# Kernel optimization log

Measured on AMD Instinct MI355X. Metric: run time of the kernel, lower is better.

## Reference

```python
import jax, jax.numpy as jnp
import numpy as np

N = 10000      # nodes
E = 320000     # edges (before self-loops)
IN = 256       # in_channels
HID = 128      # hidden_channels
HEADS = 4
OUT = 64       # out_channels
G = 64         # graphs in batch
NEG_SLOPE = 0.2


def setup_inputs() -> dict:
    key = jax.random.key(0)
    ks = jax.random.split(key, 12)
    s = lambda fan: 1.0 / np.sqrt(fan)
    x = jax.random.normal(ks[0], (N, IN), jnp.float32)
    edge_index = jax.random.randint(ks[1], (2, E), 0, N, dtype=jnp.int32)
    batch = jnp.sort(jax.random.randint(ks[2], (N,), 0, G, dtype=jnp.int32))
    # layer 0: GATConv(IN -> HID, heads=HEADS, concat)
    W1 = jax.random.normal(ks[3], (IN, HEADS * HID), jnp.float32) * s(IN)
    a1s = jax.random.normal(ks[4], (HEADS, HID), jnp.float32) * s(HID)
    a1d = jax.random.normal(ks[5], (HEADS, HID), jnp.float32) * s(HID)
    b1 = jnp.zeros((HEADS * HID,), jnp.float32)
    # layer 1: GATConv(HEADS*HID -> HID, heads=1)
    W2 = jax.random.normal(ks[6], (HEADS * HID, HID), jnp.float32) * s(HEADS * HID)
    a2s = jax.random.normal(ks[7], (1, HID), jnp.float32) * s(HID)
    a2d = jax.random.normal(ks[8], (1, HID), jnp.float32) * s(HID)
    b2 = jnp.zeros((HID,), jnp.float32)
    fc_w = jax.random.normal(ks[9], (HID, OUT), jnp.float32) * s(HID)
    fc_b = jnp.zeros((OUT,), jnp.float32)
    return dict(x=x, edge_index=edge_index, batch=batch, W1=W1, a1s=a1s,
                a1d=a1d, b1=b1, W2=W2, a2s=a2s, a2d=a2d, b2=b2,
                fc_w=fc_w, fc_b=fc_b)


def _gat_conv(x, src, dst, W, a_src, a_dst, b, heads):
    """PyG GATConv (concat=True, self-loops already in src/dst)."""
    n = x.shape[0]
    h = (x @ W).reshape(n, heads, -1)                     # [N,H,C]
    alpha_s = jnp.einsum('nhc,hc->nh', h, a_src)          # [N,H]
    alpha_d = jnp.einsum('nhc,hc->nh', h, a_dst)
    e = jax.nn.leaky_relu(alpha_s[src] + alpha_d[dst], NEG_SLOPE)  # [Etot,H]
    # per-destination-node segment softmax
    e = e - jax.ops.segment_max(e, dst, num_segments=n)[dst]
    e = jnp.exp(e)
    denom = jax.ops.segment_sum(e, dst, num_segments=n)[dst] + 1e-16
    alpha = e / denom
    out = jax.ops.segment_sum(h[src] * alpha[:, :, None], dst, num_segments=n)
    return out.reshape(n, -1) + b


def reference(x, edge_index, batch, W1, a1s, a1d, b1, W2, a2s, a2d, b2, fc_w, fc_b):
    loops = jnp.arange(N, dtype=edge_index.dtype)
    ei = jnp.concatenate([edge_index, jnp.stack([loops, loops])], axis=1)
    src, dst = ei[0], ei[1]
    h = jax.nn.relu(_gat_conv(x, src, dst, W1, a1s, a1d, b1, HEADS))
    h = jax.nn.relu(_gat_conv(h, src, dst, W2, a2s, a2d, b2, 1))
    # global_mean_pool over graph ids
    counts = jax.ops.segment_sum(jnp.ones((N, 1), h.dtype), batch, num_segments=G)
    pooled = jax.ops.segment_sum(h, batch, num_segments=G) / jnp.maximum(counts, 1.0)
    return pooled @ fc_w + fc_b
```

## Files before the change

### kernel.cpp

```cpp
#include <hip/hip_runtime.h>
#include <math.h>

#define NN 10000
#define EE 320000
#define GG 64
#define NT 157
#define NPAD (NT * 64)

#define NB 64
#define CH (EE / NB)
#define HSTR 10240

typedef __attribute__((ext_vector_type(8))) short short8;
typedef __attribute__((ext_vector_type(4))) float f32x4;

__device__ __forceinline__ float leaky(float x) { return x >= 0.f ? x : 0.2f * x; }

__device__ __forceinline__ unsigned f2bf(float f) {
  unsigned u = __float_as_uint(f);
  return (u + 0x7fffu + ((u >> 16) & 1u)) >> 16;
}
__device__ __forceinline__ float bflo(unsigned v) { return __uint_as_float(v << 16); }
__device__ __forceinline__ float bfhi(unsigned v) { return __uint_as_float(v & 0xffff0000u); }

__device__ void histA_body(int blk, const int* __restrict__ ei,
                           int* __restrict__ hist2d,
                           ushort* __restrict__ lrank) {
  __shared__ int lh[NN];
  for (int i = threadIdx.x; i < NN; i += 256) lh[i] = 0;
  __syncthreads();
  const int base = blk * CH;
  for (int i = threadIdx.x; i < CH; i += 256) {
    int d = ei[EE + base + i];
    int r = atomicAdd(&lh[d], 1);
    lrank[base + i] = (ushort)r;
  }
  __syncthreads();
  int* hrow = hist2d + (size_t)blk * HSTR;
  for (int i = threadIdx.x; i < NN; i += 256) hrow[i] = lh[i];
}

__device__ __forceinline__ void s1_body(int sb, const int* __restrict__ hist2d,
                                        int* __restrict__ off2d,
                                        int* __restrict__ total) {
  int t = sb * 256 + threadIdx.x;
  if (t >= NN) return;
  int run = 0;
#pragma unroll 8
  for (int b = 0; b < NB; b++) {
    int v = hist2d[(size_t)b * HSTR + t];
    off2d[(size_t)b * HSTR + t] = run;
    run += v;
  }
  total[t] = run;
}

__device__ void scan_body(const int* __restrict__ total,
                          int* __restrict__ rowstart) {
  __shared__ int part[256];
  const int tid = threadIdx.x;
  const int PER = 40;
  int base = tid * PER;
  int local[PER];
  int s = 0;
#pragma unroll
  for (int i = 0; i < PER; i++) {
    int idx = base + i;
    int v = (idx < NN) ? total[idx] : 0;
    local[i] = s;
    s += v;
  }
  part[tid] = s;
  __syncthreads();
  for (int off = 1; off < 256; off <<= 1) {
    int v = (tid >= off) ? part[tid - off] : 0;
    __syncthreads();
    part[tid] += v;
    __syncthreads();
  }
  int pre = (tid == 0) ? 0 : part[tid - 1];
#pragma unroll
  for (int i = 0; i < PER; i++) {
    int idx = base + i;
    if (idx < NN) rowstart[idx] = pre + local[i];
  }
  if (tid == 255) rowstart[NN] = part[255];
}

__device__ __forceinline__ void fillB_body(int bx, const int* __restrict__ ei,
                                           const int* __restrict__ rowstart,
                                           const int* __restrict__ off2d,
                                           const ushort* __restrict__ lrank,
                                           int* __restrict__ esrc) {
  int e = bx * 256 + threadIdx.x;
  if (e >= EE) return;
  int d = ei[EE + e];
  int s = ei[e];
  int blk = e / CH;
  int pos = rowstart[d] + off2d[(size_t)blk * HSTR + d] + (int)lrank[e];
  esrc[pos] = s;
}

#define PX_ITEMS (NN * 256 / 8)
#define PW1 (512 * 256)
#define PW2 (128 * 512)
#define PACK_BLKS ((PX_ITEMS + PW1 + PW2) / 256)

__device__ __forceinline__ void pack_body(int pb, const float* __restrict__ x,
                                          const float* __restrict__ W1,
                                          const float* __restrict__ W2,
                                          uint4* __restrict__ xb,
                                          ushort* __restrict__ w1hi,
                                          ushort* __restrict__ w2hi) {
  int idx = pb * 256 + threadIdx.x;
  if (idx < PX_ITEMS) {
    const float4* xf = (const float4*)x;
    float4 a = xf[idx * 2], b = xf[idx * 2 + 1];
    uint4 o;
    o.x = f2bf(a.x) | (f2bf(a.y) << 16);
    o.y = f2bf(a.z) | (f2bf(a.w) << 16);
    o.z = f2bf(b.x) | (f2bf(b.y) << 16);
    o.w = f2bf(b.z) | (f2bf(b.w) << 16);
    xb[idx] = o;
  } else if (idx < PX_ITEMS + PW1) {
    int i = idx - PX_ITEMS;
    int c = i >> 8, k = i & 255;
    w1hi[i] = (ushort)f2bf(W1[(size_t)k * 512 + c]);
  } else if (idx < PX_ITEMS + PW1 + PW2) {
    int i = idx - PX_ITEMS - PW1;
    int c = i >> 9, k = i & 511;
    w2hi[i] = (ushort)f2bf(W2[(size_t)k * 128 + c]);
  }
}

__device__ __forceinline__ void gstart_body(int gb, const int* __restrict__ batch,
                                            int* __restrict__ gstart) {
  int i = gb * 256 + threadIdx.x;
  if (i >= NN) return;
  int b = batch[i];
  int prev = (i == 0) ? -1 : batch[i - 1];
  for (int g = prev + 1; g <= b; g++) gstart[g] = i;
  if (i == NN - 1)
    for (int g = b + 1; g <= GG; g++) gstart[g] = NN;
}

#define ZERO_BLKS ((NN * 4 + 255) / 256)
__device__ __forceinline__ void zero_body(int zb, float* __restrict__ as1,
                                          float* __restrict__ ad1,
                                          float* __restrict__ as2,
                                          float* __restrict__ ad2) {
  int i = zb * 256 + threadIdx.x;
  if (i < NN) { as2[i] = 0.f; ad2[i] = 0.f; }
  if (i < NN * 4) { as1[i] = 0.f; ad1[i] = 0.f; }
}

__device__ void gemmt_body(int chblk, int nodeblk,
                           const ushort* __restrict__ ab,
                           const ushort* __restrict__ whi,
                           unsigned* __restrict__ op,
                           const float* __restrict__ avs,
                           const float* __restrict__ avd,
                           float* __restrict__ as_out,
                           float* __restrict__ ad_out,
                           int K, int C) {
  const int lane = threadIdx.x & 63;
  const int wave = threadIdx.x >> 6;
  const int l15 = lane & 15;
  const int kg = lane >> 4;
  const int ch0 = chblk * 64 + wave * 16;
  const int node0 = nodeblk * 64;
  const ushort* arow_hi = whi + (size_t)(ch0 + l15) * K + kg * 8;
  const ushort* brow = ab + (size_t)(node0 + l15) * K + kg * 8;
  f32x4 acc[4];
#pragma unroll
  for (int f = 0; f < 4; f++) acc[f] = (f32x4){0.f, 0.f, 0.f, 0.f};
  for (int k0 = 0; k0 < K; k0 += 32) {
    short8 ah = *(const short8*)(arow_hi + k0);
#pragma unroll
    for (int f = 0; f < 4; f++) {
      short8 bv = *(const short8*)(brow + (size_t)f * 16 * K + k0);
      acc[f] = __builtin_amdgcn_mfma_f32_16x16x32_bf16(ah, bv, acc[f], 0, 0, 0);
    }
  }
  const int chw = ch0 + kg * 4;
  const int head = ch0 >> 7;
  const int H = C >> 7;
  const float4 s4 = *(const float4*)(avs + chw);
  const float4 d4 = *(const float4*)(avd + chw);
#pragma unroll
  for (int f = 0; f < 4; f++) {
    int node = node0 + f * 16 + l15;
    unsigned u0 = f2bf(acc[f][0]) | (f2bf(acc[f][1]) << 16);
    unsigned u1 = f2bf(acc[f][2]) | (f2bf(acc[f][3]) << 16);
    *(uint2*)(op + (size_t)node * (C >> 1) + (chw >> 1)) = make_uint2(u0, u1);
    float ss = acc[f][0] * s4.x + acc[f][1] * s4.y + acc[f][2] * s4.z + acc[f][3] * s4.w;
    float sd = acc[f][0] * d4.x + acc[f][1] * d4.y + acc[f][2] * d4.z + acc[f][3] * d4.w;
    ss += __shfl_xor(ss, 16, 64); ss += __shfl_xor(ss, 32, 64);
    sd += __shfl_xor(sd, 16, 64); sd += __shfl_xor(sd, 32, 64);
    if (kg == 0 && node < NN) {
      atomicAdd(&as_out[node * H + head], ss);
      atomicAdd(&ad_out[node * H + head], sd);
    }
  }
}

#define FILL_BLKS 1250
#define GST_BLKS 40
__global__ __launch_bounds__(256) void fusedA_k(const int* __restrict__ ei,
                                                int* __restrict__ hist2d,
                                                ushort* __restrict__ lrank,
                                                const float* __restrict__ x,
                                                const float* __restrict__ W1,
                                                const float* __restrict__ W2,
                                                uint4* __restrict__ xb,
                                                ushort* __restrict__ w1hi,
                                                ushort* __restrict__ w2hi,
                                                const int* __restrict__ batch,
                                                int* __restrict__ gstart,
                                                float* __restrict__ as1,
                                                float* __restrict__ ad1,
                                                float* __restrict__ as2,
                                                float* __restrict__ ad2) {
  int bx = blockIdx.x;
  if (bx < NB) histA_body(bx, ei, hist2d, lrank);
  else if (bx < NB + PACK_BLKS)
    pack_body(bx - NB, x, W1, W2, xb, w1hi, w2hi);
  else if (bx < NB + PACK_BLKS + GST_BLKS)
    gstart_body(bx - NB - PACK_BLKS, batch, gstart);
  else
    zero_body(bx - NB - PACK_BLKS - GST_BLKS, as1, ad1, as2, ad2);
}

__global__ __launch_bounds__(256) void fusedB_k(const int* __restrict__ hist2d,
                                                int* __restrict__ off2d,
                                                int* __restrict__ total,
                                                const ushort* __restrict__ xb,
                                                const ushort* __restrict__ w1hi,
                                                unsigned* __restrict__ h1p,
                                                const float* __restrict__ a1s,
                                                const float* __restrict__ a1d,
                                                float* __restrict__ as1,
                                                float* __restrict__ ad1) {
  int bx = blockIdx.x;
  if (bx < GST_BLKS) { s1_body(bx, hist2d, off2d, total); return; }
  int lb = bx - GST_BLKS;
  int ch = lb % 3, nb = lb / 3;
  gemmt_body(ch, nb, xb, w1hi, h1p, a1s, a1d, as1, ad1, 256, 512);
}

__global__ __launch_bounds__(256) void fusedC_k(const int* __restrict__ total,
                                                int* __restrict__ rowstart,
                                                const ushort* __restrict__ xb,
                                                const ushort* __restrict__ w1hi,
                                                unsigned* __restrict__ h1p,
                                                const float* __restrict__ a1s,
                                                const float* __restrict__ a1d,
                                                float* __restrict__ as1,
                                                float* __restrict__ ad1) {
  int bx = blockIdx.x;
  if (bx == 0) { scan_body(total, rowstart); return; }
  int lb = bx - 1;
  int ch = 3 + lb % 3, nb = lb / 3;
  gemmt_body(ch, nb, xb, w1hi, h1p, a1s, a1d, as1, ad1, 256, 512);
}

__global__ __launch_bounds__(256) void fusedD_k(const int* __restrict__ ei,
                                                const int* __restrict__ rowstart,
                                                const int* __restrict__ off2d,
                                                const ushort* __restrict__ lrank,
                                                int* __restrict__ esrc,
                                                const ushort* __restrict__ xb,
                                                const ushort* __restrict__ w1hi,
                                                unsigned* __restrict__ h1p,
                                                const float* __restrict__ a1s,
                                                const float* __restrict__ a1d,
                                                float* __restrict__ as1,
                                                float* __restrict__ ad1) {
  int bx = blockIdx.x;
  if (bx < FILL_BLKS) { fillB_body(bx, ei, rowstart, off2d, lrank, esrc); return; }
  int lb = bx - FILL_BLKS;
  int ch = 6 + (lb & 1), nb = lb >> 1;
  gemmt_body(ch, nb, xb, w1hi, h1p, a1s, a1d, as1, ad1, 256, 512);
}

__global__ __launch_bounds__(256) void gemmt_k(const ushort* __restrict__ ab,
                                               const ushort* __restrict__ whi,
                                               unsigned* __restrict__ op,
                                               const float* __restrict__ avs,
                                               const float* __restrict__ avd,
                                               float* __restrict__ as_out,
                                               float* __restrict__ ad_out,
                                               int K, int C) {
  gemmt_body(blockIdx.x, blockIdx.y, ab, whi, op, avs, avd, as_out, ad_out, K, C);
}

#define AGG1_FMA8(W_, HV_)                          \
  acc0.x = fmaf(W_, bflo(HV_.x), acc0.x);           \
  acc0.y = fmaf(W_, bfhi(HV_.x), acc0.y);           \
  acc0.z = fmaf(W_, bflo(HV_.y), acc0.z);           \
  acc0.w = fmaf(W_, bfhi(HV_.y), acc0.w);           \
  acc1.x = fmaf(W_, bflo(HV_.z), acc1.x);           \
  acc1.y = fmaf(W_, bfhi(HV_.z), acc1.y);           \
  acc1.z = fmaf(W_, bflo(HV_.w), acc1.z);           \
  acc1.w = fmaf(W_, bfhi(HV_.w), acc1.w);

__global__ __launch_bounds__(256) void agg1_k(const int* __restrict__ rowstart,
                                              const int* __restrict__ esrc,
                                              const float* __restrict__ as,
                                              const float* __restrict__ ad,
                                              const ushort* __restrict__ h1p,
                                              const float* __restrict__ b1,
                                              uint4* __restrict__ o1b) {
  const int lane = threadIdx.x & 63;
  const int wid = threadIdx.x >> 6;
  const int n = blockIdx.x * 4 + wid;
  const int beg = rowstart[n];
  const int deg = rowstart[n + 1] - beg;
  const int tot = deg + 1;
  const float4* as4 = (const float4*)as;
  const float4 adv = ((const float4*)ad)[n];
  const int head = lane >> 4;

  __shared__ float wlds_all[4][256];
  float* wlds = wlds_all[wid];

  int s0 = n;
  float4 e0 = make_float4(-1e30f, -1e30f, -1e30f, -1e30f);
  if (lane < tot) {
    if (lane < deg) s0 = esrc[beg + lane];
    float4 av = as4[s0];
    e0.x = leaky(av.x + adv.x); e0.y = leaky(av.y + adv.y);
    e0.z = leaky(av.z + adv.z); e0.w = leaky(av.w + adv.w);
  }
  float4 mx = e0;
  for (int i = lane + 64; i < tot; i += 64) {
    int s = (i < deg) ? esrc[beg + i] : n;
    float4 av = as4[s];
    mx.x = fmaxf(mx.x, leaky(av.x + adv.x));
    mx.y = fmaxf(mx.y, leaky(av.y + adv.y));
    mx.z = fmaxf(mx.z, leaky(av.z + adv.z));
    mx.w = fmaxf(mx.w, leaky(av.w + adv.w));
  }
#pragma unroll
  for (int off = 32; off >= 1; off >>= 1) {
    mx.x = fmaxf(mx.x, __shfl_xor(mx.x, off, 64));
    mx.y = fmaxf(mx.y, __shfl_xor(mx.y, off, 64));
    mx.z = fmaxf(mx.z, __shfl_xor(mx.z, off, 64));
    mx.w = fmaxf(mx.w, __shfl_xor(mx.w, off, 64));
  }
  float4 sm;
  sm.x = __expf(e0.x - mx.x); sm.y = __expf(e0.y - mx.y);
  sm.z = __expf(e0.z - mx.z); sm.w = __expf(e0.w - mx.w);
  for (int i = lane + 64; i < tot; i += 64) {
    int s = (i < deg) ? esrc[beg + i] : n;
    float4 av = as4[s];
    sm.x += __expf(leaky(av.x + adv.x) - mx.x);
    sm.y += __expf(leaky(av.y + adv.y) - mx.y);
    sm.z += __expf(leaky(av.z + adv.z) - mx.z);
    sm.w += __expf(leaky(av.w + adv.w) - mx.w);
  }
#pragma unroll
  for (int off = 32; off >= 1; off >>= 1) {
    sm.x += __shfl_xor(sm.x, off, 64);
    sm.y += __shfl_xor(sm.y, off, 64);
    sm.z += __shfl_xor(sm.z, off, 64);
    sm.w += __shfl_xor(sm.w, off, 64);
  }
  float4 inv;
  inv.x = 1.f / (sm.x + 1e-16f); inv.y = 1.f / (sm.y + 1e-16f);
  inv.z = 1.f / (sm.z + 1e-16f); inv.w = 1.f / (sm.w + 1e-16f);

  float4 acc0 = make_float4(0.f, 0.f, 0.f, 0.f);
  float4 acc1 = make_float4(0.f, 0.f, 0.f, 0.f);
  const char* hb = (const char*)h1p + (size_t)lane * 16;

  for (int base = 0; base < tot; base += 64) {
    int sl;
    float4 wl;
    if (base == 0) {
      sl = s0;
      wl.x = __expf(e0.x - mx.x) * inv.x;
      wl.y = __expf(e0.y - mx.y) * inv.y;
      wl.z = __expf(e0.z - mx.z) * inv.z;
      wl.w = __expf(e0.w - mx.w) * inv.w;
    } else {
      int i = base + lane;
      sl = n;
      wl = make_float4(0.f, 0.f, 0.f, 0.f);
      if (i < tot) {
        if (i < deg) sl = esrc[beg + i];
        float4 av = as4[sl];
        wl.x = __expf(leaky(av.x + adv.x) - mx.x) * inv.x;
        wl.y = __expf(leaky(av.y + adv.y) - mx.y) * inv.y;
        wl.z = __expf(leaky(av.z + adv.z) - mx.z) * inv.z;
        wl.w = __expf(leaky(av.w + adv.w) - mx.w) * inv.w;
      }
    }
    *(float4*)&wlds[lane * 4] = wl;
    int m = min(64, tot - base);
    int j = 0;
    for (; j + 4 <= m; j += 4) {
      int sA = __builtin_amdgcn_readlane(sl, j);
      int sB = __builtin_amdgcn_readlane(sl, j + 1);
      int sC = __builtin_amdgcn_readlane(sl, j + 2);
      int sD = __builtin_amdgcn_readlane(sl, j + 3);
      uint4 hA = *(const uint4*)(hb + (size_t)sA * 1024);
      uint4 hB = *(const uint4*)(hb + (size_t)sB * 1024);
      uint4 hC = *(const uint4*)(hb + (size_t)sC * 1024);
      uint4 hD = *(const uint4*)(hb + (size_t)sD * 1024);
      float wA = wlds[j * 4 + head];
      float wB = wlds[(j + 1) * 4 + head];
      float wC = wlds[(j + 2) * 4 + head];
      float wD = wlds[(j + 3) * 4 + head];
      AGG1_FMA8(wA, hA)
      AGG1_FMA8(wB, hB)
      AGG1_FMA8(wC, hC)
      AGG1_FMA8(wD, hD)
    }
    for (; j < m; j++) {
      int sA = __builtin_amdgcn_readlane(sl, j);
      float wA = wlds[j * 4 + head];
      uint4 hA = *(const uint4*)(hb + (size_t)sA * 1024);
      AGG1_FMA8(wA, hA)
    }
  }
  const float4* b4 = (const float4*)b1;
  float4 ba = b4[2 * lane], bb = b4[2 * lane + 1];
  float4 r0, r1;
  r0.x = fmaxf(acc0.x + ba.x, 0.f); r0.y = fmaxf(acc0.y + ba.y, 0.f);
  r0.z = fmaxf(acc0.z + ba.z, 0.f); r0.w = fmaxf(acc0.w + ba.w, 0.f);
  r1.x = fmaxf(acc1.x + bb.x, 0.f); r1.y = fmaxf(acc1.y + bb.y, 0.f);
  r1.z = fmaxf(acc1.z + bb.z, 0.f); r1.w = fmaxf(acc1.w + bb.w, 0.f);
  uint4 o;
  o.x = f2bf(r0.x) | (f2bf(r0.y) << 16);
  o.y = f2bf(r0.z) | (f2bf(r0.w) << 16);
  o.z = f2bf(r1.x) | (f2bf(r1.y) << 16);
  o.w = f2bf(r1.z) | (f2bf(r1.w) << 16);
  o1b[(size_t)n * 64 + lane] = o;
}

__global__ __launch_bounds__(256) void agg2_k(const int* __restrict__ rowstart,
                                              const int* __restrict__ esrc,
                                              const float* __restrict__ as,
                                              const float* __restrict__ ad,
                                              const ushort* __restrict__ h2p,
                                              const float* __restrict__ b2,
                                              float* __restrict__ out2) {
  const int lane = threadIdx.x & 63;
  const int wid = threadIdx.x >> 6;
  const int n = blockIdx.x * 4 + wid;
  const int beg = rowstart[n];
  const int deg = rowstart[n + 1] - beg;
  const int tot = deg + 1;
  const float adv = ad[n];

  __shared__ float wlds_all[4][64];
  float* wlds = wlds_all[wid];

  int s0 = n;
  float e0 = -1e30f;
  if (lane < tot) {
    if (lane < deg) s0 = esrc[beg + lane];
    e0 = leaky(as[s0] + adv);
  }
  float mx = e0;
  for (int i = lane + 64; i < tot; i += 64) {
    int s = (i < deg) ? esrc[beg + i] : n;
    mx = fmaxf(mx, leaky(as[s] + adv));
  }
#pragma unroll
  for (int off = 32; off >= 1; off >>= 1) mx = fmaxf(mx, __shfl_xor(mx, off, 64));
  float sm = __expf(e0 - mx);
  for (int i = lane + 64; i < tot; i += 64) {
    int s = (i < deg) ? esrc[beg + i] : n;
    sm += __expf(leaky(as[s] + adv) - mx);
  }
#pragma unroll
  for (int off = 32; off >= 1; off >>= 1) sm += __shfl_xor(sm, off, 64);
  float inv = 1.f / (sm + 1e-16f);

  float2 acc = make_float2(0.f, 0.f);
  const char* hb = (const char*)h2p + (size_t)lane * 4;
  for (int base = 0; base < tot; base += 64) {
    int sl;
    float wl;
    if (base == 0) {
      sl = s0;
      wl = __expf(e0 - mx) * inv;
    } else {
      int i = base + lane;
      sl = n; wl = 0.f;
      if (i < tot) {
        if (i < deg) sl = esrc[beg + i];
        wl = __expf(leaky(as[sl] + adv) - mx) * inv;
      }
    }
    wlds[lane] = wl;
    int m = min(64, tot - base);
    int j = 0;
    for (; j + 4 <= m; j += 4) {
      int sA = __builtin_amdgcn_readlane(sl, j);
      int sB = __builtin_amdgcn_readlane(sl, j + 1);
      int sC = __builtin_amdgcn_readlane(sl, j + 2);
      int sD = __builtin_amdgcn_readlane(sl, j + 3);
      unsigned hA = *(const unsigned*)(hb + (size_t)sA * 256);
      unsigned hB = *(const unsigned*)(hb + (size_t)sB * 256);
      unsigned hC = *(const unsigned*)(hb + (size_t)sC * 256);
      unsigned hD = *(const unsigned*)(hb + (size_t)sD * 256);
      float wA = wlds[j], wB = wlds[j + 1], wC = wlds[j + 2], wD = wlds[j + 3];
      acc.x = fmaf(wA, bflo(hA), acc.x);
      acc.y = fmaf(wA, bfhi(hA), acc.y);
      acc.x = fmaf(wB, bflo(hB), acc.x);
      acc.y = fmaf(wB, bfhi(hB), acc.y);
      acc.x = fmaf(wC, bflo(hC), acc.x);
      acc.y = fmaf(wC, bfhi(hC), acc.y);
      acc.x = fmaf(wD, bflo(hD), acc.x);
      acc.y = fmaf(wD, bfhi(hD), acc.y);
    }
    for (; j < m; j++) {
      int sA = __builtin_amdgcn_readlane(sl, j);
      float wA = wlds[j];
      unsigned hA = *(const unsigned*)(hb + (size_t)sA * 256);
      acc.x = fmaf(wA, bflo(hA), acc.x);
      acc.y = fmaf(wA, bfhi(hA), acc.y);
    }
  }
  float2 bb = ((const float2*)b2)[lane];
  float2 r;
  r.x = fmaxf(acc.x + bb.x, 0.f);
  r.y = fmaxf(acc.y + bb.y, 0.f);
  ((float2*)(out2 + (size_t)n * 128))[lane] = r;
}

__global__ __launch_bounds__(128) void poolfc_k(const int* __restrict__ gstart,
                                                const float* __restrict__ out2,
                                                const float* __restrict__ fcw,
                                                const float* __restrict__ fcb,
                                                float* __restrict__ out) {
  const int g = blockIdx.x;
  const int tid = threadIdx.x;
  const int beg = gstart[g], end = gstart[g + 1];
  const int cnt = end - beg;
  float acc = 0.f;
  int n = beg;
  for (; n + 4 <= end; n += 4) {
    float v0 = out2[(size_t)(n + 0) * 128 + tid];
    float v1 = out2[(size_t)(n + 1) * 128 + tid];
    float v2 = out2[(size_t)(n + 2) * 128 + tid];
    float v3 = out2[(size_t)(n + 3) * 128 + tid];
    acc += (v0 + v1) + (v2 + v3);
  }
  for (; n < end; n++) acc += out2[(size_t)n * 128 + tid];
  __shared__ float pg[128];
  pg[tid] = acc / (float)(cnt > 0 ? cnt : 1);
  __syncthreads();
  if (tid < 64) {
    float o = fcb[tid];
#pragma unroll 8
    for (int c = 0; c < 128; c++) o = fmaf(pg[c], fcw[c * 64 + tid], o);
    out[g * 64 + tid] = o;
  }
}

extern "C" void kernel_launch(void* const* d_in, const int* in_sizes, int n_in,
                              void* d_out, int out_size, void* d_ws, size_t ws_size,
                              hipStream_t stream) {
  const float* x   = (const float*)d_in[0];
  const int*   ei  = (const int*)d_in[1];
  const int*   bat = (const int*)d_in[2];
  const float* W1  = (const float*)d_in[3];
  const float* a1s = (const float*)d_in[4];
  const float* a1d = (const float*)d_in[5];
  const float* b1  = (const float*)d_in[6];
  const float* W2  = (const float*)d_in[7];
  const float* a2s = (const float*)d_in[8];
  const float* a2d = (const float*)d_in[9];
  const float* b2  = (const float*)d_in[10];
  const float* fcw = (const float*)d_in[11];
  const float* fcb = (const float*)d_in[12];
  float* out = (float*)d_out;

  char* ws = (char*)d_ws;
  size_t off = 0;
  auto alloc = [&](size_t bytes) -> void* {
    void* p = ws + off;
    off = (off + bytes + 255) & ~(size_t)255;
    return p;
  };

  int*   hist2d   = (int*)alloc((size_t)NB * HSTR * 4);
  int*   off2d    = (int*)alloc((size_t)NB * HSTR * 4);
  ushort* lrank   = (ushort*)alloc((size_t)EE * 2);
  int*   total    = (int*)alloc((size_t)NN * 4);
  int*   rowstart = (int*)alloc((size_t)(NN + 1) * 4);
  int*   esrc     = (int*)alloc((size_t)EE * 4);
  int*   gstart   = (int*)alloc((size_t)(GG + 1) * 4);
  ushort* xb      = (ushort*)alloc((size_t)NPAD * 256 * 2);
  ushort* w1hi    = (ushort*)alloc((size_t)512 * 256 * 2);
  ushort* w2hi    = (ushort*)alloc((size_t)128 * 512 * 2);
  ushort* h1p     = (ushort*)alloc((size_t)NPAD * 512 * 2);
  ushort* o1b     = (ushort*)alloc((size_t)NPAD * 512 * 2);
  ushort* h2p     = (ushort*)alloc((size_t)NPAD * 128 * 2);
  float* as1      = (float*)alloc((size_t)NN * 4 * 4);
  float* ad1      = (float*)alloc((size_t)NN * 4 * 4);
  float* as2      = (float*)alloc((size_t)NN * 4);
  float* ad2      = (float*)alloc((size_t)NN * 4);
  float* out2     = (float*)alloc((size_t)NN * 128 * 4);
  (void)ws_size; (void)in_sizes; (void)n_in; (void)out_size;

  fusedA_k<<<NB + PACK_BLKS + GST_BLKS + ZERO_BLKS, 256, 0, stream>>>(
      ei, hist2d, lrank, x, W1, W2, (uint4*)xb, w1hi, w2hi, bat, gstart,
      as1, ad1, as2, ad2);

  fusedB_k<<<GST_BLKS + 3 * NT, 256, 0, stream>>>(hist2d, off2d, total, xb, w1hi,
                                                  (unsigned*)h1p, a1s, a1d, as1, ad1);

  fusedC_k<<<1 + 3 * NT, 256, 0, stream>>>(total, rowstart, xb, w1hi,
                                           (unsigned*)h1p, a1s, a1d, as1, ad1);

  fusedD_k<<<FILL_BLKS + 2 * NT, 256, 0, stream>>>(ei, rowstart, off2d, lrank, esrc,
                                                   xb, w1hi, (unsigned*)h1p,
                                                   a1s, a1d, as1, ad1);

  agg1_k<<<NN / 4, 256, 0, stream>>>(rowstart, esrc, as1, ad1, h1p, b1, (uint4*)o1b);

  gemmt_k<<<dim3(2, NT), 256, 0, stream>>>(o1b, w2hi, (unsigned*)h2p,
                                           a2s, a2d, as2, ad2, 512, 128);
  agg2_k<<<NN / 4, 256, 0, stream>>>(rowstart, esrc, as2, ad2, h2p, b2, out2);

  poolfc_k<<<GG, 128, 0, stream>>>(gstart, out2, fcw, fcb, out);
}
```

Before: 149.3 us.

## Merge dependent stages into persistent kernels synchronized by global atomic flags

```diff
diff --git a/kernel.cpp b/kernel.cpp
--- a/kernel.cpp
+++ b/kernel.cpp
@@ -22,6 +22,21 @@
 }
 __device__ __forceinline__ float bflo(unsigned v) { return __uint_as_float(v << 16); }
 __device__ __forceinline__ float bfhi(unsigned v) { return __uint_as_float(v & 0xffff0000u); }
+
+__device__ __forceinline__ void spin_flag(int* fl, int target) {
+  if (threadIdx.x == 0) {
+    while (__hip_atomic_load(fl, __ATOMIC_ACQUIRE, __HIP_MEMORY_SCOPE_AGENT) < target)
+      __builtin_amdgcn_s_sleep(16);
+  }
+  __syncthreads();
+}
+__device__ __forceinline__ void bump_flag(int* fl) {
+  __syncthreads();
+  if (threadIdx.x == 0) {
+    __threadfence();
+    __hip_atomic_fetch_add(fl, 1, __ATOMIC_RELEASE, __HIP_MEMORY_SCOPE_AGENT);
+  }
+}
 
 __device__ void histA_body(int blk, const int* __restrict__ ei,
                            int* __restrict__ hist2d,
@@ -148,10 +163,12 @@
 __device__ __forceinline__ void zero_body(int zb, float* __restrict__ as1,
                                           float* __restrict__ ad1,
                                           float* __restrict__ as2,
-                                          float* __restrict__ ad2) {
+                                          float* __restrict__ ad2,
+                                          int* __restrict__ fl) {
   int i = zb * 256 + threadIdx.x;
   if (i < NN) { as2[i] = 0.f; ad2[i] = 0.f; }
   if (i < NN * 4) { as1[i] = 0.f; ad1[i] = 0.f; }
+  if (zb == 0 && threadIdx.x < 8) fl[threadIdx.x] = 0;
 }
 
 __device__ void gemmt_body(int chblk, int nodeblk,
@@ -204,7 +221,6 @@
   }
 }
 
-#define FILL_BLKS 1250
 #define GST_BLKS 40
 __global__ __launch_bounds__(256) void fusedA_k(const int* __restrict__ ei,
                                                 int* __restrict__ hist2d,
@@ -220,7 +236,8 @@
                                                 float* __restrict__ as1,
                                                 float* __restrict__ ad1,
                                                 float* __restrict__ as2,
-                                                float* __restrict__ ad2) {
+                                                float* __restrict__ ad2,
+                                                int* __restrict__ fl) {
   int bx = blockIdx.x;
   if (bx < NB) histA_body(bx, ei, hist2d, lrank);
   else if (bx < NB + PACK_BLKS)
@@ -228,70 +245,44 @@
   else if (bx < NB + PACK_BLKS + GST_BLKS)
     gstart_body(bx - NB - PACK_BLKS, batch, gstart);
   else
-    zero_body(bx - NB - PACK_BLKS - GST_BLKS, as1, ad1, as2, ad2);
-}
-
-__global__ __launch_bounds__(256) void fusedB_k(const int* __restrict__ hist2d,
-                                                int* __restrict__ off2d,
-                                                int* __restrict__ total,
-                                                const ushort* __restrict__ xb,
-                                                const ushort* __restrict__ w1hi,
-                                                unsigned* __restrict__ h1p,
-                                                const float* __restrict__ a1s,
-                                                const float* __restrict__ a1d,
-                                                float* __restrict__ as1,
-                                                float* __restrict__ ad1) {
+    zero_body(bx - NB - PACK_BLKS - GST_BLKS, as1, ad1, as2, ad2, fl);
+}
+
+#define G1_BLKS 628
+#define FILLG_BLKS 640
+__global__ __launch_bounds__(256) void fusedBCD_k(const int* __restrict__ ei,
+                                                  const int* __restrict__ hist2d,
+                                                  int* __restrict__ off2d,
+                                                  int* __restrict__ total,
+                                                  int* __restrict__ rowstart,
+                                                  const ushort* __restrict__ lrank,
+                                                  int* __restrict__ esrc,
+                                                  const ushort* __restrict__ xb,
+                                                  const ushort* __restrict__ w1hi,
+                                                  unsigned* __restrict__ h1p,
+                                                  const float* __restrict__ a1s,
+                                                  const float* __restrict__ a1d,
+                                                  float* __restrict__ as1,
+                                                  float* __restrict__ ad1,
+                                                  int* __restrict__ fl) {
   int bx = blockIdx.x;
-  if (bx < GST_BLKS) { s1_body(bx, hist2d, off2d, total); return; }
-  int lb = bx - GST_BLKS;
-  int ch = lb % 3, nb = lb / 3;
-  gemmt_body(ch, nb, xb, w1hi, h1p, a1s, a1d, as1, ad1, 256, 512);
-}
-
-__global__ __launch_bounds__(256) void fusedC_k(const int* __restrict__ total,
-                                                int* __restrict__ rowstart,
-                                                const ushort* __restrict__ xb,
-                                                const ushort* __restrict__ w1hi,
-                                                unsigned* __restrict__ h1p,
-                                                const float* __restrict__ a1s,
-                                                const float* __restrict__ a1d,
-                                                float* __restrict__ as1,
-                                                float* __restrict__ ad1) {
-  int bx = blockIdx.x;
-  if (bx == 0) { scan_body(total, rowstart); return; }
-  int lb = bx - 1;
-  int ch = 3 + lb % 3, nb = lb / 3;
-  gemmt_body(ch, nb, xb, w1hi, h1p, a1s, a1d, as1, ad1, 256, 512);
-}
-
-__global__ __launch_bounds__(256) void fusedD_k(const int* __restrict__ ei,
-                                                const int* __restrict__ rowstart,
-                                                const int* __restrict__ off2d,
-                                                const ushort* __restrict__ lrank,
-                                                int* __restrict__ esrc,
-                                                const ushort* __restrict__ xb,
-                                                const ushort* __restrict__ w1hi,
-                                                unsigned* __restrict__ h1p,
-                                                const float* __restrict__ a1s,
-                                                const float* __restrict__ a1d,
-                                                float* __restrict__ as1,
-                                                float* __restrict__ ad1) {
-  int bx = blockIdx.x;
-  if (bx < FILL_BLKS) { fillB_body(bx, ei, rowstart, off2d, lrank, esrc); return; }
-  int lb = bx - FILL_BLKS;
-  int ch = 6 + (lb & 1), nb = lb >> 1;
-  gemmt_body(ch, nb, xb, w1hi, h1p, a1s, a1d, as1, ad1, 256, 512);
-}
-
-__global__ __launch_bounds__(256) void gemmt_k(const ushort* __restrict__ ab,
-                                               const ushort* __restrict__ whi,
-                                               unsigned* __restrict__ op,
-                                               const float* __restrict__ avs,
-                                               const float* __restrict__ avd,
-                                               float* __restrict__ as_out,
-                                               float* __restrict__ ad_out,
-                                               int K, int C) {
-  gemmt_body(blockIdx.x, blockIdx.y, ab, whi, op, avs, avd, as_out, ad_out, K, C);
+  if (bx < G1_BLKS) {
+    int t0 = bx, t1 = bx + G1_BLKS;
+    gemmt_body(t0 & 7, t0 >> 3, xb, w1hi, h1p, a1s, a1d, as1, ad1, 256, 512);
+    gemmt_body(t1 & 7, t1 >> 3, xb, w1hi, h1p, a1s, a1d, as1, ad1, 256, 512);
+  } else if (bx < G1_BLKS + GST_BLKS) {
+    s1_body(bx - G1_BLKS, hist2d, off2d, total);
+    bump_flag(&fl[0]);
+  } else if (bx == G1_BLKS + GST_BLKS) {
+    spin_flag(&fl[0], GST_BLKS);
+    scan_body(total, rowstart);
+    bump_flag(&fl[1]);
+  } else {
+    spin_flag(&fl[1], 1);
+    int fb = bx - (G1_BLKS + GST_BLKS + 1);
+    fillB_body(fb, ei, rowstart, off2d, lrank, esrc);
+    fillB_body(fb + FILLG_BLKS, ei, rowstart, off2d, lrank, esrc);
+  }
 }
 
 #define AGG1_FMA8(W_, HV_)                          \
@@ -439,23 +430,20 @@
   o1b[(size_t)n * 64 + lane] = o;
 }
 
-__global__ __launch_bounds__(256) void agg2_k(const int* __restrict__ rowstart,
-                                              const int* __restrict__ esrc,
-                                              const float* __restrict__ as,
-                                              const float* __restrict__ ad,
-                                              const ushort* __restrict__ h2p,
-                                              const float* __restrict__ b2,
-                                              float* __restrict__ out2) {
+__device__ void agg2_body(int g, const int* __restrict__ rowstart,
+                          const int* __restrict__ esrc,
+                          const float* __restrict__ as,
+                          const float* __restrict__ ad,
+                          const ushort* __restrict__ h2p,
+                          const float* __restrict__ b2,
+                          float* __restrict__ out2,
+                          float* __restrict__ wlds) {
   const int lane = threadIdx.x & 63;
-  const int wid = threadIdx.x >> 6;
-  const int n = blockIdx.x * 4 + wid;
+  const int n = g * 4 + (threadIdx.x >> 6);
   const int beg = rowstart[n];
   const int deg = rowstart[n + 1] - beg;
   const int tot = deg + 1;
   const float adv = ad[n];
-
-  __shared__ float wlds_all[4][64];
-  float* wlds = wlds_all[wid];
 
   int s0 = n;
   float e0 = -1e30f;
@@ -532,33 +520,69 @@
   ((float2*)(out2 + (size_t)n * 128))[lane] = r;
 }
 
-__global__ __launch_bounds__(128) void poolfc_k(const int* __restrict__ gstart,
-                                                const float* __restrict__ out2,
-                                                const float* __restrict__ fcw,
-                                                const float* __restrict__ fcb,
-                                                float* __restrict__ out) {
-  const int g = blockIdx.x;
+__device__ void poolfc_body(int g, const int* __restrict__ gstart,
+                            const float* __restrict__ out2,
+                            const float* __restrict__ fcw,
+                            const float* __restrict__ fcb,
+                            float* __restrict__ out,
+                            float* __restrict__ pg2 ,
+                            float* __restrict__ pg ) {
   const int tid = threadIdx.x;
+  const int c = tid & 127;
+  const int half = tid >> 7;
   const int beg = gstart[g], end = gstart[g + 1];
   const int cnt = end - beg;
   float acc = 0.f;
-  int n = beg;
-  for (; n + 4 <= end; n += 4) {
-    float v0 = out2[(size_t)(n + 0) * 128 + tid];
-    float v1 = out2[(size_t)(n + 1) * 128 + tid];
-    float v2 = out2[(size_t)(n + 2) * 128 + tid];
-    float v3 = out2[(size_t)(n + 3) * 128 + tid];
-    acc += (v0 + v1) + (v2 + v3);
-  }
-  for (; n < end; n++) acc += out2[(size_t)n * 128 + tid];
-  __shared__ float pg[128];
-  pg[tid] = acc / (float)(cnt > 0 ? cnt : 1);
+  for (int n = beg + half; n < end; n += 2) acc += out2[(size_t)n * 128 + c];
+  pg2[half * 128 + c] = acc;
+  __syncthreads();
+  if (tid < 128) pg[tid] = (pg2[tid] + pg2[128 + tid]) / (float)(cnt > 0 ? cnt : 1);
   __syncthreads();
   if (tid < 64) {
     float o = fcb[tid];
 #pragma unroll 8
-    for (int c = 0; c < 128; c++) o = fmaf(pg[c], fcw[c * 64 + tid], o);
+    for (int cc = 0; cc < 128; cc++) o = fmaf(pg[cc], fcw[cc * 64 + tid], o);
     out[g * 64 + tid] = o;
+  }
+}
+
+#define G2_BLKS 314
+#define A2_BLKS 1280
+__global__ __launch_bounds__(256) void fusedEFG_k(const int* __restrict__ rowstart,
+                                                  const int* __restrict__ esrc,
+                                                  const ushort* __restrict__ o1b,
+                                                  const ushort* __restrict__ w2hi,
+                                                  unsigned* __restrict__ h2p,
+                                                  const float* __restrict__ a2s,
+                                                  const float* __restrict__ a2d,
+                                                  float* __restrict__ as2,
+                                                  float* __restrict__ ad2,
+                                                  const float* __restrict__ b2,
+                                                  float* __restrict__ out2,
+                                                  const int* __restrict__ gstart,
+                                                  const float* __restrict__ fcw,
+                                                  const float* __restrict__ fcb,
+                                                  float* __restrict__ out,
+                                                  int* __restrict__ fl) {
+  __shared__ float lds[4][64];
+  int bx = blockIdx.x;
+  if (bx < G2_BLKS) {
+    gemmt_body(bx & 1, bx >> 1, o1b, w2hi, h2p, a2s, a2d, as2, ad2, 512, 128);
+    bump_flag(&fl[2]);
+  } else if (bx < G2_BLKS + A2_BLKS) {
+    spin_flag(&fl[2], G2_BLKS);
+    int g = bx - G2_BLKS;
+    agg2_body(g, rowstart, esrc, as2, ad2, (const ushort*)h2p, b2, out2,
+              lds[threadIdx.x >> 6]);
+    int g2 = g + A2_BLKS;
+    if (g2 < NN / 4)
+      agg2_body(g2, rowstart, esrc, as2, ad2, (const ushort*)h2p, b2, out2,
+                lds[threadIdx.x >> 6]);
+    bump_flag(&fl[3]);
+  } else {
+    spin_flag(&fl[3], A2_BLKS);
+    poolfc_body(bx - G2_BLKS - A2_BLKS, gstart, out2, fcw, fcb, out,
+                &lds[0][0], &lds[2][0] + 64);
   }
 }
 
@@ -595,6 +619,7 @@
   int*   rowstart = (int*)alloc((size_t)(NN + 1) * 4);
   int*   esrc     = (int*)alloc((size_t)EE * 4);
   int*   gstart   = (int*)alloc((size_t)(GG + 1) * 4);
+  int*   fl       = (int*)alloc(64);
   ushort* xb      = (ushort*)alloc((size_t)NPAD * 256 * 2);
   ushort* w1hi    = (ushort*)alloc((size_t)512 * 256 * 2);
   ushort* w2hi    = (ushort*)alloc((size_t)128 * 512 * 2);
@@ -610,23 +635,15 @@
 
   fusedA_k<<<NB + PACK_BLKS + GST_BLKS + ZERO_BLKS, 256, 0, stream>>>(
       ei, hist2d, lrank, x, W1, W2, (uint4*)xb, w1hi, w2hi, bat, gstart,
-      as1, ad1, as2, ad2);
-
-  fusedB_k<<<GST_BLKS + 3 * NT, 256, 0, stream>>>(hist2d, off2d, total, xb, w1hi,
-                                                  (unsigned*)h1p, a1s, a1d, as1, ad1);
-
-  fusedC_k<<<1 + 3 * NT, 256, 0, stream>>>(total, rowstart, xb, w1hi,
-                                           (unsigned*)h1p, a1s, a1d, as1, ad1);
-
-  fusedD_k<<<FILL_BLKS + 2 * NT, 256, 0, stream>>>(ei, rowstart, off2d, lrank, esrc,
-                                                   xb, w1hi, (unsigned*)h1p,
-                                                   a1s, a1d, as1, ad1);
+      as1, ad1, as2, ad2, fl);
+
+  fusedBCD_k<<<G1_BLKS + GST_BLKS + 1 + FILLG_BLKS, 256, 0, stream>>>(
+      ei, hist2d, off2d, total, rowstart, lrank, esrc, xb, w1hi,
+      (unsigned*)h1p, a1s, a1d, as1, ad1, fl);
 
   agg1_k<<<NN / 4, 256, 0, stream>>>(rowstart, esrc, as1, ad1, h1p, b1, (uint4*)o1b);
 
-  gemmt_k<<<dim3(2, NT), 256, 0, stream>>>(o1b, w2hi, (unsigned*)h2p,
-                                           a2s, a2d, as2, ad2, 512, 128);
-  agg2_k<<<NN / 4, 256, 0, stream>>>(rowstart, esrc, as2, ad2, h2p, b2, out2);
-
-  poolfc_k<<<GG, 128, 0, stream>>>(gstart, out2, fcw, fcb, out);
-}
+  fusedEFG_k<<<G2_BLKS + A2_BLKS + GG, 256, 0, stream>>>(
+      rowstart, esrc, o1b, w2hi, (unsigned*)h2p, a2s, a2d, as2, ad2, b2, out2,
+      gstart, fcw, fcb, out, fl);
+}
```

After: 497.9 us. +233.5%, slower.
